# Performance work log

Hardware: AMD Instinct MI355X
Metric: run time of the kernel (lower is better)

## Reference

```python
import jax, jax.numpy as jnp
import numpy as np

N = 100000   # nodes
E = 1600000  # edges
F_IN = 64    # n_features
H = 32       # hidden_size
OUT = 1      # output_size


def _lin(k, fan_in, fan_out):
    return (jax.random.normal(k, (fan_in, fan_out), jnp.float32) / np.sqrt(fan_in)).astype(jnp.float32)


def setup_inputs() -> dict:
    key = jax.random.key(0)
    ks = jax.random.split(key, 16)
    x = jax.random.normal(ks[0], (N, F_IN), jnp.float32)
    edge_index = jax.random.randint(ks[1], (2, E), 0, N, dtype=jnp.int64)
    # guarantee current_node (=0) has outgoing edges so the legal-move mask is non-empty
    edge_index = edge_index.at[0, :64].set(0)
    edge_attr = jax.random.uniform(ks[2], (E,), jnp.float32)
    return {
        "x": x, "edge_index": edge_index, "edge_attr": edge_attr, "current_node": 0,
        # conv_in: GraphConv(F_IN -> H)
        "Win_rel": _lin(ks[3], F_IN, H), "bin_rel": jnp.zeros((H,), jnp.float32), "Win_root": _lin(ks[4], F_IN, H),
        # conv_hidden: GraphConv(H -> H)
        "Wh_rel": _lin(ks[5], H, H), "bh_rel": jnp.zeros((H,), jnp.float32), "Wh_root": _lin(ks[6], H, H),
        # policy_conv: GraphConv(H -> OUT)
        "Wp_rel": _lin(ks[7], H, OUT), "bp_rel": jnp.zeros((OUT,), jnp.float32), "Wp_root": _lin(ks[8], H, OUT),
        # value_conv: GraphConv(H -> OUT)
        "Wv_rel": _lin(ks[9], H, OUT), "bv_rel": jnp.zeros((OUT,), jnp.float32), "Wv_root": _lin(ks[10], H, OUT),
    }


def _graph_conv(h, src, dst, ew, W_rel, b_rel, W_root):
    # PyG GraphConv: out_i = W_root h_i + W_rel * sum_{j->i} e_ji * h_j + b
    msg = h[src] * ew[:, None]                              # [E, d] gather + scale
    agg = jax.ops.segment_sum(msg, dst, num_segments=N)      # [N, d] scatter-add
    return agg @ W_rel + b_rel + h @ W_root


def reference(x, edge_index, edge_attr, current_node,
              Win_rel, bin_rel, Win_root,
              Wh_rel, bh_rel, Wh_root,
              Wp_rel, bp_rel, Wp_root,
              Wv_rel, bv_rel, Wv_root):
    src, dst = edge_index[0], edge_index[1]
    h = jax.nn.relu(_graph_conv(x, src, dst, edge_attr, Win_rel, bin_rel, Win_root))
    h = jax.nn.relu(_graph_conv(h, src, dst, edge_attr, Wh_rel, bh_rel, Wh_root))
    p = _graph_conv(h, src, dst, edge_attr, Wp_rel, bp_rel, Wp_root)  # [N, 1]
    v = _graph_conv(h, src, dst, edge_attr, Wv_rel, bv_rel, Wv_root)  # [N, 1]
    # illegal_moves_mask: 1 for nodes directly reachable from current_node
    hit = (src == current_node).astype(jnp.float32)
    mask = (jnp.zeros((N,), jnp.float32).at[dst].add(hit) > 0).astype(jnp.float32)
    p_m = mask * p.T                                   # [1, N]
    p_m = jnp.where(p_m == 0, -jnp.inf, p_m)
    p_soft = jax.nn.softmax(p_m, axis=1)
    v_m = mask * v.T                                   # [1, N]
    return p_soft.reshape(-1), v_m.reshape(-1)
```

## Files before the change

### kernel.cpp

```cpp
#include <hip/hip_runtime.h>
#include <hip/hip_fp16.h>
#include <cmath>

static constexpr int NN = 100000;
static constexpr int NE = 1600000;
static const size_t NW = (size_t)NN * 32;
static constexpr int SUB = 256;
static constexpr int NSUB = 391;
static constexpr int CH = 8192;
static constexpr int NCH = (NE + CH - 1) / CH;
static constexpr int BCAP = 5200;
static constexpr int CSRN = NSUB * BCAP;
static constexpr int MCAP = 4096;

__device__ __forceinline__ float ent_w(unsigned e)
{
    return __half2float(__ushort_as_half((unsigned short)(e >> 17)));
}
__device__ __forceinline__ int ent_s(unsigned e)
{
    int s = (int)(e & 0x1FFFF);
    return s < NN ? s : NN - 1;
}

__device__ __forceinline__ float4 pack8(const float* v)
{
    union { __half2 h2[4]; float4 f4; } u;
    u.h2[0] = __floats2half2_rn(v[0], v[1]);
    u.h2[1] = __floats2half2_rn(v[2], v[3]);
    u.h2[2] = __floats2half2_rn(v[4], v[5]);
    u.h2[3] = __floats2half2_rn(v[6], v[7]);
    return u.f4;
}

__global__ void __launch_bounds__(512) fused_build_mm1_k(
    const int* __restrict__ src, const int* __restrict__ dst,
    const float* __restrict__ ew, const int* __restrict__ curp,
    int* __restrict__ maskb, int* __restrict__ mcount, int* __restrict__ mlist,
    int* __restrict__ bcnt, uint2* __restrict__ buckets,
    const float* __restrict__ x, const float* __restrict__ Wrel,
    const float* __restrict__ Wroot, const float* __restrict__ bin,
    __half* __restrict__ proj1, __half* __restrict__ root1)
{
    __shared__ union {
        struct {
            uint2 sBuf[CH];
            int lhist[NSUB];
            int lpos[NSUB];
            int lstart[NSUB];
            int lbase[NSUB];
            int tscan[512];
        } s;
        struct {
            float sX[128 * 65];
            float sW[64 * 68];
        } m;
    } u;

    int t = threadIdx.x;
    int bid = blockIdx.x;

    if (bid < NCH) {
        for (int i = t; i < NSUB; i += 512) { u.s.lhist[i] = 0; u.s.lpos[i] = 0; }
        __syncthreads();
        int c0 = bid * CH;
        int cur = curp[0];
        uint2 rent[CH / 512];
        int rb[CH / 512];
#pragma unroll
        for (int it = 0; it < CH / 512; ++it) {
            int e = c0 + it * 512 + t;
            rb[it] = -1;
            if (e < NE) {
                int d = dst[e];
                int sv = src[e];
                if ((unsigned)d < (unsigned)NN) {
                    rb[it] = d >> 8;
                    unsigned bits = __half_as_ushort(__float2half(ew[e]));
                    rent[it].x = ((unsigned)sv & 0x1FFFF) | (bits << 17);
                    rent[it].y = (unsigned)d;
                    atomicAdd(&u.s.lhist[rb[it]], 1);
                    if (sv == cur) {
                        if (atomicExch(maskb + d, 1) == 0) {
                            int idx = atomicAdd(mcount, 1);
                            if (idx < MCAP) mlist[idx] = d;
                        }
                    }
                }
            }
        }
        __syncthreads();
        int v = (t < NSUB) ? u.s.lhist[t] : 0;
        u.s.tscan[t] = v;
        __syncthreads();
        for (int sh = 1; sh < 512; sh <<= 1) {
            int xv = u.s.tscan[t];
            int a = (t >= sh) ? u.s.tscan[t - sh] : 0;
            __syncthreads();
            u.s.tscan[t] = xv + a;
            __syncthreads();
        }
        if (t < NSUB) {
            u.s.lstart[t] = u.s.tscan[t] - v;
            u.s.lbase[t] = (v > 0) ? atomicAdd(&bcnt[t], v) : 0;
        }
        __syncthreads();
#pragma unroll
        for (int it = 0; it < CH / 512; ++it) {
            if (rb[it] >= 0) {
                int p = atomicAdd(&u.s.lpos[rb[it]], 1);
                u.s.sBuf[u.s.lstart[rb[it]] + p] = rent[it];
            }
        }
        __syncthreads();
        int total = u.s.lstart[NSUB - 1] + u.s.lhist[NSUB - 1];
        for (int j = t; j < total; j += 512) {
            uint2 en = u.s.sBuf[j];
            int b = (int)(en.y >> 8);
            if (b >= NSUB) b = NSUB - 1;
            unsigned pos = (unsigned)(u.s.lbase[b] + (j - u.s.lstart[b]));
            if (pos < (unsigned)BCAP) buckets[(size_t)b * BCAP + pos] = en;
        }
    } else {
        int mb = bid - NCH;
        for (int i = t; i < 64 * 32; i += 512) {
            int k = i >> 5, j = i & 31;
            u.m.sW[k * 68 + j] = Wrel[i];
            u.m.sW[k * 68 + 32 + j] = Wroot[i];
        }
        int base = mb * 128;
        for (int i = t; i < 2048; i += 512) {
            int node = i >> 4;
            int k = (i & 15) * 4;
            int n = base + node;
            if (n >= NN) n = NN - 1;
            float4 v4 = *(const float4*)(x + (size_t)n * 64 + k);
            float* p = u.m.sX + node * 65 + k;
            p[0] = v4.x; p[1] = v4.y; p[2] = v4.z; p[3] = v4.w;
        }
        __syncthreads();
        int cg = t & 7;
        int ng = t >> 3;
        int c0m = 8 * cg;
        float acc[2][8] = {};
        for (int k = 0; k < 64; ++k) {
            float xv0 = u.m.sX[(2 * ng + 0) * 65 + k];
            float xv1 = u.m.sX[(2 * ng + 1) * 65 + k];
            float4 w0 = *(const float4*)(u.m.sW + k * 68 + c0m);
            float4 w1 = *(const float4*)(u.m.sW + k * 68 + c0m + 4);
            const float* wp = (const float*)&w0;
#pragma unroll
            for (int j = 0; j < 4; ++j) {
                float w = wp[j];
                acc[0][j] = fmaf(xv0, w, acc[0][j]);
                acc[1][j] = fmaf(xv1, w, acc[1][j]);
            }
            const float* wq = (const float*)&w1;
#pragma unroll
            for (int j = 0; j < 4; ++j) {
                float w = wq[j];
                acc[0][4 + j] = fmaf(xv0, w, acc[0][4 + j]);
                acc[1][4 + j] = fmaf(xv1, w, acc[1][4 + j]);
            }
        }
#pragma unroll
        for (int r = 0; r < 2; ++r) {
            int n = base + 2 * ng + r;
            if (n >= NN) break;
            if (cg < 4) {
                *(float4*)(proj1 + (size_t)n * 32 + c0m) = pack8(acc[r]);
            } else {
                int c = c0m - 32;
                float vv[8];
#pragma unroll
                for (int j = 0; j < 8; ++j) vv[j] = acc[r][j] + bin[c + j];
                *(float4*)(root1 + (size_t)n * 32 + c) = pack8(vv);
            }
        }
    }
}

__global__ void __launch_bounds__(512) sortB_k(
    const uint2* __restrict__ buckets, const int* __restrict__ bcnt,
    unsigned* __restrict__ csr4, int* __restrict__ deg, int* __restrict__ off)
{
    __shared__ uint2 sBuf[BCAP];
    __shared__ int lhist[SUB];
    __shared__ int lstart[SUB];
    __shared__ int lcur[SUB];
    __shared__ int tscan[256];
    int g = blockIdx.x, t = threadIdx.x;
    if (t < SUB) { lhist[t] = 0; lcur[t] = 0; }
    __syncthreads();
    int cnt = bcnt[g];
    if (cnt < 0) cnt = 0;
    if (cnt > BCAP) cnt = BCAP;
    const uint2* bk = buckets + (size_t)g * BCAP;
    for (int i = t; i < cnt; i += 512) {
        uint2 e = bk[i];
        sBuf[i] = e;
        atomicAdd(&lhist[e.y & (SUB - 1)], 1);
    }
    __syncthreads();
    if (t < 256) tscan[t] = lhist[t];
    __syncthreads();
    for (int s = 1; s < 256; s <<= 1) {
        int x = 0, a = 0;
        if (t < 256) { x = tscan[t]; a = (t >= s) ? tscan[t - s] : 0; }
        __syncthreads();
        if (t < 256) tscan[t] = x + a;
        __syncthreads();
    }
    if (t < 256) lstart[t] = tscan[t] - lhist[t];
    __syncthreads();
    int base = g * BCAP;
    for (int i = t; i < cnt; i += 512) {
        uint2 e = sBuf[i];
        int ld = (int)(e.y & (SUB - 1));
        int p = atomicAdd(&lcur[ld], 1);
        unsigned pos = (unsigned)(base + lstart[ld] + p);
        if (pos < (unsigned)CSRN) csr4[pos] = e.x;
    }
    if (t < SUB) {
        int n = g * SUB + t;
        if (n < NN) {
            deg[n] = lhist[t];
            off[n] = base + lstart[t];
        }
    }
}

__global__ void __launch_bounds__(256) mm2_k(
    const __half* __restrict__ h1, const float* __restrict__ Wrel,
    const float* __restrict__ Wroot, const float* __restrict__ bh,
    __half* __restrict__ proj2, __half* __restrict__ root2)
{
    __shared__ float sX[128 * 33];
    __shared__ float sW[32 * 68];
    int t = threadIdx.x;
    for (int i = t; i < 32 * 32; i += 256) {
        int k = i >> 5, j = i & 31;
        sW[k * 68 + j] = Wrel[i];
        sW[k * 68 + 32 + j] = Wroot[i];
    }
    int base = blockIdx.x * 128;
    for (int i = t; i < 512; i += 256) {
        int node = i >> 2;
        int hs = (i & 3) * 8;
        int n = base + node;
        if (n >= NN) n = NN - 1;
        float4 v = *(const float4*)(h1 + (size_t)n * 32 + hs);
        const __half2* hp = (const __half2*)&v;
        float* p = sX + node * 33 + hs;
#pragma unroll
        for (int u = 0; u < 4; ++u) {
            float2 f2 = __half22float2(hp[u]);
            p[2 * u] = f2.x;
            p[2 * u + 1] = f2.y;
        }
    }
    __syncthreads();
    int cg = t & 7;
    int ng = t >> 3;
    int c0 = 8 * cg;
    float acc[4][8] = {};
    for (int k = 0; k < 32; ++k) {
        float xv0 = sX[(4 * ng + 0) * 33 + k];
        float xv1 = sX[(4 * ng + 1) * 33 + k];
        float xv2 = sX[(4 * ng + 2) * 33 + k];
        float xv3 = sX[(4 * ng + 3) * 33 + k];
        float4 w0 = *(const float4*)(sW + k * 68 + c0);
        float4 w1 = *(const float4*)(sW + k * 68 + c0 + 4);
        const float* wp = (const float*)&w0;
#pragma unroll
        for (int j = 0; j < 4; ++j) {
            float w = wp[j];
            acc[0][j] = fmaf(xv0, w, acc[0][j]);
            acc[1][j] = fmaf(xv1, w, acc[1][j]);
            acc[2][j] = fmaf(xv2, w, acc[2][j]);
            acc[3][j] = fmaf(xv3, w, acc[3][j]);
        }
        const float* wq = (const float*)&w1;
#pragma unroll
        for (int j = 0; j < 4; ++j) {
            float w = wq[j];
            acc[0][4 + j] = fmaf(xv0, w, acc[0][4 + j]);
            acc[1][4 + j] = fmaf(xv1, w, acc[1][4 + j]);
            acc[2][4 + j] = fmaf(xv2, w, acc[2][4 + j]);
            acc[3][4 + j] = fmaf(xv3, w, acc[3][4 + j]);
        }
    }
#pragma unroll
    for (int r = 0; r < 4; ++r) {
        int n = base + 4 * ng + r;
        if (n >= NN) break;
        if (cg < 4) {
            *(float4*)(proj2 + (size_t)n * 32 + c0) = pack8(acc[r]);
        } else {
            int c = c0 - 32;
            float v[8];
#pragma unroll
            for (int j = 0; j < 8; ++j) v[j] = acc[r][j] + bh[c + j];
            *(float4*)(root2 + (size_t)n * 32 + c) = pack8(v);
        }
    }
}

__global__ void __launch_bounds__(256) agg1_v4(
    const __half* __restrict__ proj1, const __half* __restrict__ root1,
    const unsigned* __restrict__ csr4, const int* __restrict__ off,
    const int* __restrict__ deg, __half* __restrict__ h1)
{
    int t = threadIdx.x;
    int q = t & 3;
    int f0 = q * 8;
    int n = blockIdx.x * 64 + (t >> 2);
    if (n >= NN) return;
    int st = off[n];
    int dg = deg[n];
    if (st < 0) st = 0;
    if (st > CSRN) st = CSRN;
    if (dg < 0) dg = 0;
    if (dg > CSRN - st) dg = CSRN - st;
    float acc[8] = {0.f, 0.f, 0.f, 0.f, 0.f, 0.f, 0.f, 0.f};
    int i = 0;
    for (; i + 1 < dg; i += 2) {
        unsigned e0 = csr4[st + i];
        unsigned e1 = csr4[st + i + 1];
        float w0 = ent_w(e0), w1 = ent_w(e1);
        float4 r0 = *(const float4*)(proj1 + (size_t)ent_s(e0) * 32 + f0);
        float4 r1 = *(const float4*)(proj1 + (size_t)ent_s(e1) * 32 + f0);
        const __half2* h0 = (const __half2*)&r0;
        const __half2* h1p = (const __half2*)&r1;
#pragma unroll
        for (int u = 0; u < 4; ++u) {
            float2 a = __half22float2(h0[u]);
            float2 b = __half22float2(h1p[u]);
            acc[2 * u] = fmaf(w0, a.x, acc[2 * u]);
            acc[2 * u + 1] = fmaf(w0, a.y, acc[2 * u + 1]);
            acc[2 * u] = fmaf(w1, b.x, acc[2 * u]);
            acc[2 * u + 1] = fmaf(w1, b.y, acc[2 * u + 1]);
        }
    }
    if (i < dg) {
        unsigned e0 = csr4[st + i];
        float w0 = ent_w(e0);
        float4 r0 = *(const float4*)(proj1 + (size_t)ent_s(e0) * 32 + f0);
        const __half2* h0 = (const __half2*)&r0;
#pragma unroll
        for (int u = 0; u < 4; ++u) {
            float2 a = __half22float2(h0[u]);
            acc[2 * u] = fmaf(w0, a.x, acc[2 * u]);
            acc[2 * u + 1] = fmaf(w0, a.y, acc[2 * u + 1]);
        }
    }
    float4 rr = *(const float4*)(root1 + (size_t)n * 32 + f0);
    const __half2* rp = (const __half2*)&rr;
    float h[8];
#pragma unroll
    for (int u = 0; u < 4; ++u) {
        float2 f2 = __half22float2(rp[u]);
        h[2 * u] = fmaxf(acc[2 * u] + f2.x, 0.f);
        h[2 * u + 1] = fmaxf(acc[2 * u + 1] + f2.y, 0.f);
    }
    *(float4*)(h1 + (size_t)n * 32 + f0) = pack8(h);
}

__global__ void __launch_bounds__(256) agg2_v4(
    const __half* __restrict__ proj2, const __half* __restrict__ root2,
    const float* __restrict__ Wp_rel, const float* __restrict__ Wp_root,
    const float* __restrict__ bp, const float* __restrict__ Wv_rel,
    const float* __restrict__ Wv_root, const float* __restrict__ bv,
    const unsigned* __restrict__ csr4, const int* __restrict__ off,
    const int* __restrict__ deg, float2* __restrict__ pv,
    float* __restrict__ pbase, float* __restrict__ vbase,
    float* __restrict__ out_p, float* __restrict__ out_v)
{
    __shared__ float sHead[4 * 32];
    if (threadIdx.x < 32) {
        sHead[threadIdx.x] = Wp_rel[threadIdx.x];
        sHead[32 + threadIdx.x] = Wp_root[threadIdx.x];
        sHead[64 + threadIdx.x] = Wv_rel[threadIdx.x];
        sHead[96 + threadIdx.x] = Wv_root[threadIdx.x];
    }
    __syncthreads();
    int t = threadIdx.x;
    int q = t & 3;
    int f0 = q * 8;
    int n = blockIdx.x * 64 + (t >> 2);
    if (n >= NN) return;
    int st = off[n];
    int dg = deg[n];
    if (st < 0) st = 0;
    if (st > CSRN) st = CSRN;
    if (dg < 0) dg = 0;
    if (dg > CSRN - st) dg = CSRN - st;
    float acc[8] = {0.f, 0.f, 0.f, 0.f, 0.f, 0.f, 0.f, 0.f};
    int i = 0;
    for (; i + 1 < dg; i += 2) {
        unsigned e0 = csr4[st + i];
        unsigned e1 = csr4[st + i + 1];
        float w0 = ent_w(e0), w1 = ent_w(e1);
        float4 r0 = *(const float4*)(proj2 + (size_t)ent_s(e0) * 32 + f0);
        float4 r1 = *(const float4*)(proj2 + (size_t)ent_s(e1) * 32 + f0);
        const __half2* h0 = (const __half2*)&r0;
        const __half2* h1p = (const __half2*)&r1;
#pragma unroll
        for (int u = 0; u < 4; ++u) {
            float2 a = __half22float2(h0[u]);
            float2 b = __half22float2(h1p[u]);
            acc[2 * u] = fmaf(w0, a.x, acc[2 * u]);
            acc[2 * u + 1] = fmaf(w0, a.y, acc[2 * u + 1]);
            acc[2 * u] = fmaf(w1, b.x, acc[2 * u]);
            acc[2 * u + 1] = fmaf(w1, b.y, acc[2 * u + 1]);
        }
    }
    if (i < dg) {
        unsigned e0 = csr4[st + i];
        float w0 = ent_w(e0);
        float4 r0 = *(const float4*)(proj2 + (size_t)ent_s(e0) * 32 + f0);
        const __half2* h0 = (const __half2*)&r0;
#pragma unroll
        for (int u = 0; u < 4; ++u) {
            float2 a = __half22float2(h0[u]);
            acc[2 * u] = fmaf(w0, a.x, acc[2 * u]);
            acc[2 * u + 1] = fmaf(w0, a.y, acc[2 * u + 1]);
        }
    }
    float4 rr = *(const float4*)(root2 + (size_t)n * 32 + f0);
    const __half2* rp = (const __half2*)&rr;
    float h[8];
#pragma unroll
    for (int u = 0; u < 4; ++u) {
        float2 f2 = __half22float2(rp[u]);
        h[2 * u] = fmaxf(acc[2 * u] + f2.x, 0.f);
        h[2 * u + 1] = fmaxf(acc[2 * u + 1] + f2.y, 0.f);
    }
    float prv = 0.f, pov = 0.f, vrv = 0.f, vov = 0.f;
#pragma unroll
    for (int j = 0; j < 8; ++j) {
        prv = fmaf(h[j], sHead[f0 + j], prv);
        pov = fmaf(h[j], sHead[32 + f0 + j], pov);
        vrv = fmaf(h[j], sHead[64 + f0 + j], vrv);
        vov = fmaf(h[j], sHead[96 + f0 + j], vov);
    }
#pragma unroll
    for (int m = 1; m <= 2; m <<= 1) {
        prv += __shfl_xor(prv, m, 64);
        pov += __shfl_xor(pov, m, 64);
        vrv += __shfl_xor(vrv, m, 64);
        vov += __shfl_xor(vov, m, 64);
    }
    if (q == 0) {
        pv[n] = make_float2(prv, vrv);
        pbase[n] = pov + bp[0];
        vbase[n] = vov + bv[0];
        out_p[n] = 0.f;
        out_v[n] = 0.f;
    }
}

__global__ void __launch_bounds__(256) masked_softmax_k(
    const int* __restrict__ mlist, const int* __restrict__ mcount,
    const unsigned* __restrict__ csr4, const int* __restrict__ off,
    const int* __restrict__ deg, const float2* __restrict__ pv,
    const float* __restrict__ pbase, const float* __restrict__ vbase,
    float* __restrict__ out_p, float* __restrict__ out_v)
{
    __shared__ float sPm[MCAP];
    __shared__ float sV[MCAP];
    __shared__ int sN[MCAP];
    __shared__ float sMx, sSum;
    __shared__ float sred[4];
    int m = mcount[0];
    if (m > MCAP) m = MCAP;
    if (m < 0) m = 0;
    for (int idx = threadIdx.x; idx < m; idx += 256) {
        int n = mlist[idx];
        if ((unsigned)n >= (unsigned)NN) n = 0;
        sN[idx] = n;
        int st = off[n];
        int dg = deg[n];
        if (st < 0) st = 0;
        if (st > CSRN) st = CSRN;
        if (dg < 0) dg = 0;
        if (dg > CSRN - st) dg = CSRN - st;
        float pa = 0.f, va = 0.f;
        for (int i = 0; i < dg; ++i) {
            unsigned ent = csr4[st + i];
            int s = ent_s(ent);
            float w = ent_w(ent);
            float2 tv = pv[s];
            pa = fmaf(tv.x, w, pa);
            va = fmaf(tv.y, w, va);
        }
        float p = pa + pbase[n];
        sPm[idx] = (p == 0.f) ? -INFINITY : p;
        sV[idx] = va + vbase[n];
    }
    __syncthreads();
    float mx = -INFINITY;
    for (int i = threadIdx.x; i < m; i += 256) mx = fmaxf(mx, sPm[i]);
#pragma unroll
    for (int k = 32; k; k >>= 1) mx = fmaxf(mx, __shfl_xor(mx, k, 64));
    if ((threadIdx.x & 63) == 0) sred[threadIdx.x >> 6] = mx;
    __syncthreads();
    if (threadIdx.x == 0)
        sMx = fmaxf(fmaxf(sred[0], sred[1]), fmaxf(sred[2], sred[3]));
    __syncthreads();
    float sum = 0.f;
    for (int i = threadIdx.x; i < m; i += 256) {
        float x = sPm[i];
        sum += (x == -INFINITY) ? 0.f : expf(x - sMx);
    }
#pragma unroll
    for (int k = 32; k; k >>= 1) sum += __shfl_xor(sum, k, 64);
    if ((threadIdx.x & 63) == 0) sred[threadIdx.x >> 6] = sum;
    __syncthreads();
    if (threadIdx.x == 0) sSum = sred[0] + sred[1] + sred[2] + sred[3];
    __syncthreads();
    for (int idx = threadIdx.x; idx < m; idx += 256) {
        int n = sN[idx];
        float x = sPm[idx];
        out_p[n] = (x == -INFINITY) ? 0.f : expf(x - sMx) / sSum;
        out_v[n] = sV[idx];
    }
}

extern "C" void kernel_launch(void* const* d_in, const int* in_sizes, int n_in,
                              void* d_out, int out_size, void* d_ws,
                              size_t ws_size, hipStream_t stream)
{
    const float* x        = (const float*)d_in[0];
    const int*   ei       = (const int*)d_in[1];
    const float* ew       = (const float*)d_in[2];
    const int*   cur      = (const int*)d_in[3];
    const float* Win_rel  = (const float*)d_in[4];
    const float* bin_rel  = (const float*)d_in[5];
    const float* Win_root = (const float*)d_in[6];
    const float* Wh_rel   = (const float*)d_in[7];
    const float* bh_rel   = (const float*)d_in[8];
    const float* Wh_root  = (const float*)d_in[9];
    const float* Wp_rel   = (const float*)d_in[10];
    const float* bp       = (const float*)d_in[11];
    const float* Wp_root  = (const float*)d_in[12];
    const float* Wv_rel   = (const float*)d_in[13];
    const float* bv       = (const float*)d_in[14];
    const float* Wv_root  = (const float*)d_in[15];

    const int* srcA = ei;
    const int* dstA = ei + NE;

    char* w8 = (char*)d_ws;
    unsigned* csr4 = (unsigned*)w8;
    int* deg    = (int*)(csr4 + CSRN);
    int* off    = deg + NN;
    int* maskb  = off + NN;
    int* mcount = maskb + NN;
    int* bcnt   = mcount + 8;
    int* mlist  = bcnt + 400;
    __half* proj1 = (__half*)(mlist + MCAP);
    __half* root1 = proj1 + NW;
    __half* h1    = root1 + NW;
    __half* proj2 = h1 + NW;
    __half* root2 = proj2 + NW;
    float2* pv    = (float2*)(root2 + NW);
    float* pbase  = (float*)(pv + NN);
    float* vbase  = pbase + NN;
    uint2* buckets = (uint2*)(vbase + NN);

    float* out_p = (float*)d_out;
    float* out_v = out_p + NN;

    const int NB_MM    = (NN + 127) / 128;
    const int NB_AGG   = (NN + 63) / 64;
    const int NB_FUSED = NCH + NB_MM;

    hipMemsetAsync(maskb, 0, ((size_t)NN + 8 + 400) * sizeof(int), stream);

    fused_build_mm1_k<<<NB_FUSED, 512, 0, stream>>>(
        srcA, dstA, ew, cur, maskb, mcount, mlist, bcnt, buckets,
        x, Win_rel, Win_root, bin_rel, proj1, root1);
    sortB_k<<<NSUB, 512, 0, stream>>>(buckets, bcnt, csr4, deg, off);

    agg1_v4<<<NB_AGG, 256, 0, stream>>>(proj1, root1, csr4, off, deg, h1);
    mm2_k<<<NB_MM, 256, 0, stream>>>(h1, Wh_rel, Wh_root, bh_rel, proj2, root2);
    agg2_v4<<<NB_AGG, 256, 0, stream>>>(proj2, root2, Wp_rel, Wp_root, bp,
                                        Wv_rel, Wv_root, bv, csr4, off, deg,
                                        pv, pbase, vbase, out_p, out_v);
    masked_softmax_k<<<1, 256, 0, stream>>>(mlist, mcount, csr4, off, deg, pv,
                                            pbase, vbase, out_p, out_v);
}
```

Measured before the change: 248.5 us.

## Drop CSR sort; aggregate from buckets via shared-memory atomics and fuse agg1 with mm2

Removes the sortB CSR-construction kernel. The two aggregation passes now read the per-256-node buckets directly and accumulate into shared memory with atomics. Layer-1 aggregation, ReLU and the hidden-layer matmul are fused into one kernel, which drops the h1 round-trip. The masked policy/value sums are computed by a bucket-scan kernel that skips slices with no masked nodes, and the chunk size drops to 4096. The cost is heavy shared-memory atomic traffic and only 391 blocks per aggregation pass, which limits parallelism.

```diff
diff --git a/kernel.cpp b/kernel.cpp
--- a/kernel.cpp
+++ b/kernel.cpp
@@ -7,10 +7,9 @@
 static const size_t NW = (size_t)NN * 32;
 static constexpr int SUB = 256;
 static constexpr int NSUB = 391;
-static constexpr int CH = 8192;
+static constexpr int CH = 4096;
 static constexpr int NCH = (NE + CH - 1) / CH;
 static constexpr int BCAP = 5200;
-static constexpr int CSRN = NSUB * BCAP;
 static constexpr int MCAP = 4096;
 
 __device__ __forceinline__ float ent_w(unsigned e)
@@ -37,7 +36,8 @@
     const int* __restrict__ src, const int* __restrict__ dst,
     const float* __restrict__ ew, const int* __restrict__ curp,
     int* __restrict__ maskb, int* __restrict__ mcount, int* __restrict__ mlist,
-    int* __restrict__ bcnt, uint2* __restrict__ buckets,
+    int* __restrict__ mslice, int* __restrict__ bcnt,
+    uint2* __restrict__ buckets,
     const float* __restrict__ x, const float* __restrict__ Wrel,
     const float* __restrict__ Wroot, const float* __restrict__ bin,
     __half* __restrict__ proj1, __half* __restrict__ root1)
@@ -84,6 +84,7 @@
                         if (atomicExch(maskb + d, 1) == 0) {
                             int idx = atomicAdd(mcount, 1);
                             if (idx < MCAP) mlist[idx] = d;
+                            mslice[d >> 8] = 1;
                         }
                     }
                 }
@@ -180,290 +181,269 @@
     }
 }
 
-__global__ void __launch_bounds__(512) sortB_k(
+__global__ void __launch_bounds__(512) agg1_mm2_k(
     const uint2* __restrict__ buckets, const int* __restrict__ bcnt,
-    unsigned* __restrict__ csr4, int* __restrict__ deg, int* __restrict__ off)
-{
-    __shared__ uint2 sBuf[BCAP];
-    __shared__ int lhist[SUB];
-    __shared__ int lstart[SUB];
-    __shared__ int lcur[SUB];
-    __shared__ int tscan[256];
+    const __half* __restrict__ proj1, const __half* __restrict__ root1,
+    const float* __restrict__ Wrel, const float* __restrict__ Wroot,
+    const float* __restrict__ bh,
+    __half* __restrict__ proj2, __half* __restrict__ root2)
+{
+    __shared__ float acc[SUB * 33];
+    __shared__ float sW[32 * 68];
     int g = blockIdx.x, t = threadIdx.x;
-    if (t < SUB) { lhist[t] = 0; lcur[t] = 0; }
+    for (int i = t; i < SUB * 33; i += 512) acc[i] = 0.f;
+    for (int i = t; i < 32 * 32; i += 512) {
+        int k = i >> 5, j = i & 31;
+        sW[k * 68 + j] = Wrel[i];
+        sW[k * 68 + 32 + j] = Wroot[i];
+    }
     __syncthreads();
     int cnt = bcnt[g];
     if (cnt < 0) cnt = 0;
     if (cnt > BCAP) cnt = BCAP;
     const uint2* bk = buckets + (size_t)g * BCAP;
-    for (int i = t; i < cnt; i += 512) {
-        uint2 e = bk[i];
-        sBuf[i] = e;
-        atomicAdd(&lhist[e.y & (SUB - 1)], 1);
-    }
-    __syncthreads();
-    if (t < 256) tscan[t] = lhist[t];
-    __syncthreads();
-    for (int s = 1; s < 256; s <<= 1) {
-        int x = 0, a = 0;
-        if (t < 256) { x = tscan[t]; a = (t >= s) ? tscan[t - s] : 0; }
-        __syncthreads();
-        if (t < 256) tscan[t] = x + a;
-        __syncthreads();
-    }
-    if (t < 256) lstart[t] = tscan[t] - lhist[t];
-    __syncthreads();
-    int base = g * BCAP;
-    for (int i = t; i < cnt; i += 512) {
-        uint2 e = sBuf[i];
-        int ld = (int)(e.y & (SUB - 1));
-        int p = atomicAdd(&lcur[ld], 1);
-        unsigned pos = (unsigned)(base + lstart[ld] + p);
-        if (pos < (unsigned)CSRN) csr4[pos] = e.x;
-    }
-    if (t < SUB) {
-        int n = g * SUB + t;
+    int q = t & 3, f0 = q * 8;
+    int i = t >> 2;
+    for (; i + 128 < cnt; i += 256) {
+        uint2 e0 = bk[i];
+        uint2 e1 = bk[i + 128];
+        float w0 = ent_w(e0.x), w1 = ent_w(e1.x);
+        float4 r0 = *(const float4*)(proj1 + (size_t)ent_s(e0.x) * 32 + f0);
+        float4 r1 = *(const float4*)(proj1 + (size_t)ent_s(e1.x) * 32 + f0);
+        float* a0 = acc + (int)(e0.y & 255) * 33 + f0;
+        float* a1 = acc + (int)(e1.y & 255) * 33 + f0;
+        const __half2* h0 = (const __half2*)&r0;
+        const __half2* h1p = (const __half2*)&r1;
+#pragma unroll
+        for (int u2 = 0; u2 < 4; ++u2) {
+            float2 a = __half22float2(h0[u2]);
+            atomicAdd(a0 + 2 * u2, w0 * a.x);
+            atomicAdd(a0 + 2 * u2 + 1, w0 * a.y);
+        }
+#pragma unroll
+        for (int u2 = 0; u2 < 4; ++u2) {
+            float2 b = __half22float2(h1p[u2]);
+            atomicAdd(a1 + 2 * u2, w1 * b.x);
+            atomicAdd(a1 + 2 * u2 + 1, w1 * b.y);
+        }
+    }
+    if (i < cnt) {
+        uint2 e0 = bk[i];
+        float w0 = ent_w(e0.x);
+        float4 r0 = *(const float4*)(proj1 + (size_t)ent_s(e0.x) * 32 + f0);
+        float* a0 = acc + (int)(e0.y & 255) * 33 + f0;
+        const __half2* h0 = (const __half2*)&r0;
+#pragma unroll
+        for (int u2 = 0; u2 < 4; ++u2) {
+            float2 a = __half22float2(h0[u2]);
+            atomicAdd(a0 + 2 * u2, w0 * a.x);
+            atomicAdd(a0 + 2 * u2 + 1, w0 * a.y);
+        }
+    }
+    __syncthreads();
+    {
+        int l = t >> 1, fb = (t & 1) * 16;
+        int n = g * SUB + l;
         if (n < NN) {
-            deg[n] = lhist[t];
-            off[n] = base + lstart[t];
-        }
-    }
-}
-
-__global__ void __launch_bounds__(256) mm2_k(
-    const __half* __restrict__ h1, const float* __restrict__ Wrel,
-    const float* __restrict__ Wroot, const float* __restrict__ bh,
-    __half* __restrict__ proj2, __half* __restrict__ root2)
-{
-    __shared__ float sX[128 * 33];
-    __shared__ float sW[32 * 68];
-    int t = threadIdx.x;
-    for (int i = t; i < 32 * 32; i += 256) {
-        int k = i >> 5, j = i & 31;
-        sW[k * 68 + j] = Wrel[i];
-        sW[k * 68 + 32 + j] = Wroot[i];
-    }
-    int base = blockIdx.x * 128;
-    for (int i = t; i < 512; i += 256) {
-        int node = i >> 2;
-        int hs = (i & 3) * 8;
-        int n = base + node;
-        if (n >= NN) n = NN - 1;
-        float4 v = *(const float4*)(h1 + (size_t)n * 32 + hs);
-        const __half2* hp = (const __half2*)&v;
-        float* p = sX + node * 33 + hs;
-#pragma unroll
-        for (int u = 0; u < 4; ++u) {
-            float2 f2 = __half22float2(hp[u]);
-            p[2 * u] = f2.x;
-            p[2 * u + 1] = f2.y;
-        }
-    }
-    __syncthreads();
-    int cg = t & 7;
-    int ng = t >> 3;
-    int c0 = 8 * cg;
-    float acc[4][8] = {};
+            float4 ra = *(const float4*)(root1 + (size_t)n * 32 + fb);
+            float4 rb = *(const float4*)(root1 + (size_t)n * 32 + fb + 8);
+            const __half2* pa = (const __half2*)&ra;
+            const __half2* pb = (const __half2*)&rb;
+            float* ap = acc + l * 33 + fb;
+#pragma unroll
+            for (int u2 = 0; u2 < 4; ++u2) {
+                float2 f2 = __half22float2(pa[u2]);
+                ap[2 * u2] = fmaxf(ap[2 * u2] + f2.x, 0.f);
+                ap[2 * u2 + 1] = fmaxf(ap[2 * u2 + 1] + f2.y, 0.f);
+            }
+#pragma unroll
+            for (int u2 = 0; u2 < 4; ++u2) {
+                float2 f2 = __half22float2(pb[u2]);
+                ap[8 + 2 * u2] = fmaxf(ap[8 + 2 * u2] + f2.x, 0.f);
+                ap[8 + 2 * u2 + 1] = fmaxf(ap[8 + 2 * u2 + 1] + f2.y, 0.f);
+            }
+        }
+    }
+    __syncthreads();
+    int cg = t & 7, ng = t >> 3, c0 = 8 * cg;
+    float a2[4][8] = {};
     for (int k = 0; k < 32; ++k) {
-        float xv0 = sX[(4 * ng + 0) * 33 + k];
-        float xv1 = sX[(4 * ng + 1) * 33 + k];
-        float xv2 = sX[(4 * ng + 2) * 33 + k];
-        float xv3 = sX[(4 * ng + 3) * 33 + k];
+        float x0 = acc[(4 * ng + 0) * 33 + k];
+        float x1 = acc[(4 * ng + 1) * 33 + k];
+        float x2 = acc[(4 * ng + 2) * 33 + k];
+        float x3 = acc[(4 * ng + 3) * 33 + k];
         float4 w0 = *(const float4*)(sW + k * 68 + c0);
         float4 w1 = *(const float4*)(sW + k * 68 + c0 + 4);
         const float* wp = (const float*)&w0;
 #pragma unroll
         for (int j = 0; j < 4; ++j) {
             float w = wp[j];
-            acc[0][j] = fmaf(xv0, w, acc[0][j]);
-            acc[1][j] = fmaf(xv1, w, acc[1][j]);
-            acc[2][j] = fmaf(xv2, w, acc[2][j]);
-            acc[3][j] = fmaf(xv3, w, acc[3][j]);
+            a2[0][j] = fmaf(x0, w, a2[0][j]);
+            a2[1][j] = fmaf(x1, w, a2[1][j]);
+            a2[2][j] = fmaf(x2, w, a2[2][j]);
+            a2[3][j] = fmaf(x3, w, a2[3][j]);
         }
         const float* wq = (const float*)&w1;
 #pragma unroll
         for (int j = 0; j < 4; ++j) {
             float w = wq[j];
-            acc[0][4 + j] = fmaf(xv0, w, acc[0][4 + j]);
-            acc[1][4 + j] = fmaf(xv1, w, acc[1][4 + j]);
-            acc[2][4 + j] = fmaf(xv2, w, acc[2][4 + j]);
-            acc[3][4 + j] = fmaf(xv3, w, acc[3][4 + j]);
+            a2[0][4 + j] = fmaf(x0, w, a2[0][4 + j]);
+            a2[1][4 + j] = fmaf(x1, w, a2[1][4 + j]);
+            a2[2][4 + j] = fmaf(x2, w, a2[2][4 + j]);
+            a2[3][4 + j] = fmaf(x3, w, a2[3][4 + j]);
         }
     }
 #pragma unroll
     for (int r = 0; r < 4; ++r) {
-        int n = base + 4 * ng + r;
+        int n = g * SUB + 4 * ng + r;
         if (n >= NN) break;
         if (cg < 4) {
-            *(float4*)(proj2 + (size_t)n * 32 + c0) = pack8(acc[r]);
+            *(float4*)(proj2 + (size_t)n * 32 + c0) = pack8(a2[r]);
         } else {
             int c = c0 - 32;
-            float v[8];
-#pragma unroll
-            for (int j = 0; j < 8; ++j) v[j] = acc[r][j] + bh[c + j];
-            *(float4*)(root2 + (size_t)n * 32 + c) = pack8(v);
-        }
-    }
-}
-
-__global__ void __launch_bounds__(256) agg1_v4(
-    const __half* __restrict__ proj1, const __half* __restrict__ root1,
-    const unsigned* __restrict__ csr4, const int* __restrict__ off,
-    const int* __restrict__ deg, __half* __restrict__ h1)
-{
-    int t = threadIdx.x;
-    int q = t & 3;
-    int f0 = q * 8;
-    int n = blockIdx.x * 64 + (t >> 2);
-    if (n >= NN) return;
-    int st = off[n];
-    int dg = deg[n];
-    if (st < 0) st = 0;
-    if (st > CSRN) st = CSRN;
-    if (dg < 0) dg = 0;
-    if (dg > CSRN - st) dg = CSRN - st;
-    float acc[8] = {0.f, 0.f, 0.f, 0.f, 0.f, 0.f, 0.f, 0.f};
-    int i = 0;
-    for (; i + 1 < dg; i += 2) {
-        unsigned e0 = csr4[st + i];
-        unsigned e1 = csr4[st + i + 1];
-        float w0 = ent_w(e0), w1 = ent_w(e1);
-        float4 r0 = *(const float4*)(proj1 + (size_t)ent_s(e0) * 32 + f0);
-        float4 r1 = *(const float4*)(proj1 + (size_t)ent_s(e1) * 32 + f0);
-        const __half2* h0 = (const __half2*)&r0;
-        const __half2* h1p = (const __half2*)&r1;
-#pragma unroll
-        for (int u = 0; u < 4; ++u) {
-            float2 a = __half22float2(h0[u]);
-            float2 b = __half22float2(h1p[u]);
-            acc[2 * u] = fmaf(w0, a.x, acc[2 * u]);
-            acc[2 * u + 1] = fmaf(w0, a.y, acc[2 * u + 1]);
-            acc[2 * u] = fmaf(w1, b.x, acc[2 * u]);
-            acc[2 * u + 1] = fmaf(w1, b.y, acc[2 * u + 1]);
-        }
-    }
-    if (i < dg) {
-        unsigned e0 = csr4[st + i];
-        float w0 = ent_w(e0);
-        float4 r0 = *(const float4*)(proj1 + (size_t)ent_s(e0) * 32 + f0);
-        const __half2* h0 = (const __half2*)&r0;
-#pragma unroll
-        for (int u = 0; u < 4; ++u) {
-            float2 a = __half22float2(h0[u]);
-            acc[2 * u] = fmaf(w0, a.x, acc[2 * u]);
-            acc[2 * u + 1] = fmaf(w0, a.y, acc[2 * u + 1]);
-        }
-    }
-    float4 rr = *(const float4*)(root1 + (size_t)n * 32 + f0);
-    const __half2* rp = (const __half2*)&rr;
-    float h[8];
-#pragma unroll
-    for (int u = 0; u < 4; ++u) {
-        float2 f2 = __half22float2(rp[u]);
-        h[2 * u] = fmaxf(acc[2 * u] + f2.x, 0.f);
-        h[2 * u + 1] = fmaxf(acc[2 * u + 1] + f2.y, 0.f);
-    }
-    *(float4*)(h1 + (size_t)n * 32 + f0) = pack8(h);
-}
-
-__global__ void __launch_bounds__(256) agg2_v4(
+            float vv[8];
+#pragma unroll
+            for (int j = 0; j < 8; ++j) vv[j] = a2[r][j] + bh[c + j];
+            *(float4*)(root2 + (size_t)n * 32 + c) = pack8(vv);
+        }
+    }
+}
+
+__global__ void __launch_bounds__(512) agg2_k(
+    const uint2* __restrict__ buckets, const int* __restrict__ bcnt,
     const __half* __restrict__ proj2, const __half* __restrict__ root2,
     const float* __restrict__ Wp_rel, const float* __restrict__ Wp_root,
     const float* __restrict__ bp, const float* __restrict__ Wv_rel,
     const float* __restrict__ Wv_root, const float* __restrict__ bv,
-    const unsigned* __restrict__ csr4, const int* __restrict__ off,
-    const int* __restrict__ deg, float2* __restrict__ pv,
-    float* __restrict__ pbase, float* __restrict__ vbase,
-    float* __restrict__ out_p, float* __restrict__ out_v)
-{
+    float2* __restrict__ pv, float* __restrict__ pbase,
+    float* __restrict__ vbase, float* __restrict__ out_p,
+    float* __restrict__ out_v)
+{
+    __shared__ float acc[SUB * 33];
     __shared__ float sHead[4 * 32];
-    if (threadIdx.x < 32) {
-        sHead[threadIdx.x] = Wp_rel[threadIdx.x];
-        sHead[32 + threadIdx.x] = Wp_root[threadIdx.x];
-        sHead[64 + threadIdx.x] = Wv_rel[threadIdx.x];
-        sHead[96 + threadIdx.x] = Wv_root[threadIdx.x];
-    }
-    __syncthreads();
-    int t = threadIdx.x;
-    int q = t & 3;
-    int f0 = q * 8;
-    int n = blockIdx.x * 64 + (t >> 2);
-    if (n >= NN) return;
-    int st = off[n];
-    int dg = deg[n];
-    if (st < 0) st = 0;
-    if (st > CSRN) st = CSRN;
-    if (dg < 0) dg = 0;
-    if (dg > CSRN - st) dg = CSRN - st;
-    float acc[8] = {0.f, 0.f, 0.f, 0.f, 0.f, 0.f, 0.f, 0.f};
-    int i = 0;
-    for (; i + 1 < dg; i += 2) {
-        unsigned e0 = csr4[st + i];
-        unsigned e1 = csr4[st + i + 1];
-        float w0 = ent_w(e0), w1 = ent_w(e1);
-        float4 r0 = *(const float4*)(proj2 + (size_t)ent_s(e0) * 32 + f0);
-        float4 r1 = *(const float4*)(proj2 + (size_t)ent_s(e1) * 32 + f0);
+    int g = blockIdx.x, t = threadIdx.x;
+    for (int i = t; i < SUB * 33; i += 512) acc[i] = 0.f;
+    if (t < 32) {
+        sHead[t] = Wp_rel[t];
+        sHead[32 + t] = Wp_root[t];
+        sHead[64 + t] = Wv_rel[t];
+        sHead[96 + t] = Wv_root[t];
+    }
+    __syncthreads();
+    int cnt = bcnt[g];
+    if (cnt < 0) cnt = 0;
+    if (cnt > BCAP) cnt = BCAP;
+    const uint2* bk = buckets + (size_t)g * BCAP;
+    int q = t & 3, f0 = q * 8;
+    int i = t >> 2;
+    for (; i + 128 < cnt; i += 256) {
+        uint2 e0 = bk[i];
+        uint2 e1 = bk[i + 128];
+        float w0 = ent_w(e0.x), w1 = ent_w(e1.x);
+        float4 r0 = *(const float4*)(proj2 + (size_t)ent_s(e0.x) * 32 + f0);
+        float4 r1 = *(const float4*)(proj2 + (size_t)ent_s(e1.x) * 32 + f0);
+        float* a0 = acc + (int)(e0.y & 255) * 33 + f0;
+        float* a1 = acc + (int)(e1.y & 255) * 33 + f0;
         const __half2* h0 = (const __half2*)&r0;
         const __half2* h1p = (const __half2*)&r1;
 #pragma unroll
-        for (int u = 0; u < 4; ++u) {
-            float2 a = __half22float2(h0[u]);
-            float2 b = __half22float2(h1p[u]);
-            acc[2 * u] = fmaf(w0, a.x, acc[2 * u]);
-            acc[2 * u + 1] = fmaf(w0, a.y, acc[2 * u + 1]);
-            acc[2 * u] = fmaf(w1, b.x, acc[2 * u]);
-            acc[2 * u + 1] = fmaf(w1, b.y, acc[2 * u + 1]);
-        }
-    }
-    if (i < dg) {
-        unsigned e0 = csr4[st + i];
-        float w0 = ent_w(e0);
-        float4 r0 = *(const float4*)(proj2 + (size_t)ent_s(e0) * 32 + f0);
+        for (int u2 = 0; u2 < 4; ++u2) {
+            float2 a = __half22float2(h0[u2]);
+            atomicAdd(a0 + 2 * u2, w0 * a.x);
+            atomicAdd(a0 + 2 * u2 + 1, w0 * a.y);
+        }
+#pragma unroll
+        for (int u2 = 0; u2 < 4; ++u2) {
+            float2 b = __half22float2(h1p[u2]);
+            atomicAdd(a1 + 2 * u2, w1 * b.x);
+            atomicAdd(a1 + 2 * u2 + 1, w1 * b.y);
+        }
+    }
+    if (i < cnt) {
+        uint2 e0 = bk[i];
+        float w0 = ent_w(e0.x);
+        float4 r0 = *(const float4*)(proj2 + (size_t)ent_s(e0.x) * 32 + f0);
+        float* a0 = acc + (int)(e0.y & 255) * 33 + f0;
         const __half2* h0 = (const __half2*)&r0;
 #pragma unroll
-        for (int u = 0; u < 4; ++u) {
-            float2 a = __half22float2(h0[u]);
-            acc[2 * u] = fmaf(w0, a.x, acc[2 * u]);
-            acc[2 * u + 1] = fmaf(w0, a.y, acc[2 * u + 1]);
-        }
-    }
-    float4 rr = *(const float4*)(root2 + (size_t)n * 32 + f0);
-    const __half2* rp = (const __half2*)&rr;
-    float h[8];
-#pragma unroll
-    for (int u = 0; u < 4; ++u) {
-        float2 f2 = __half22float2(rp[u]);
-        h[2 * u] = fmaxf(acc[2 * u] + f2.x, 0.f);
-        h[2 * u + 1] = fmaxf(acc[2 * u + 1] + f2.y, 0.f);
-    }
-    float prv = 0.f, pov = 0.f, vrv = 0.f, vov = 0.f;
-#pragma unroll
-    for (int j = 0; j < 8; ++j) {
-        prv = fmaf(h[j], sHead[f0 + j], prv);
-        pov = fmaf(h[j], sHead[32 + f0 + j], pov);
-        vrv = fmaf(h[j], sHead[64 + f0 + j], vrv);
-        vov = fmaf(h[j], sHead[96 + f0 + j], vov);
-    }
-#pragma unroll
-    for (int m = 1; m <= 2; m <<= 1) {
-        prv += __shfl_xor(prv, m, 64);
-        pov += __shfl_xor(pov, m, 64);
-        vrv += __shfl_xor(vrv, m, 64);
-        vov += __shfl_xor(vov, m, 64);
-    }
-    if (q == 0) {
-        pv[n] = make_float2(prv, vrv);
-        pbase[n] = pov + bp[0];
-        vbase[n] = vov + bv[0];
-        out_p[n] = 0.f;
-        out_v[n] = 0.f;
+        for (int u2 = 0; u2 < 4; ++u2) {
+            float2 a = __half22float2(h0[u2]);
+            atomicAdd(a0 + 2 * u2, w0 * a.x);
+            atomicAdd(a0 + 2 * u2 + 1, w0 * a.y);
+        }
+    }
+    __syncthreads();
+    int l = t >> 1, fb = (t & 1) * 16;
+    int n = g * SUB + l;
+    if (n < NN) {
+        float4 ra = *(const float4*)(root2 + (size_t)n * 32 + fb);
+        float4 rb = *(const float4*)(root2 + (size_t)n * 32 + fb + 8);
+        const __half2* pa = (const __half2*)&ra;
+        const __half2* pb = (const __half2*)&rb;
+        const float* ap = acc + l * 33 + fb;
+        float h[16];
+#pragma unroll
+        for (int u2 = 0; u2 < 4; ++u2) {
+            float2 f2 = __half22float2(pa[u2]);
+            h[2 * u2] = fmaxf(ap[2 * u2] + f2.x, 0.f);
+            h[2 * u2 + 1] = fmaxf(ap[2 * u2 + 1] + f2.y, 0.f);
+        }
+#pragma unroll
+        for (int u2 = 0; u2 < 4; ++u2) {
+            float2 f2 = __half22float2(pb[u2]);
+            h[8 + 2 * u2] = fmaxf(ap[8 + 2 * u2] + f2.x, 0.f);
+            h[8 + 2 * u2 + 1] = fmaxf(ap[8 + 2 * u2 + 1] + f2.y, 0.f);
+        }
+        float pr = 0.f, po = 0.f, vr = 0.f, vo = 0.f;
+#pragma unroll
+        for (int j = 0; j < 16; ++j) {
+            int f = fb + j;
+            pr = fmaf(h[j], sHead[f], pr);
+            po = fmaf(h[j], sHead[32 + f], po);
+            vr = fmaf(h[j], sHead[64 + f], vr);
+            vo = fmaf(h[j], sHead[96 + f], vo);
+        }
+        pr += __shfl_xor(pr, 1, 64);
+        po += __shfl_xor(po, 1, 64);
+        vr += __shfl_xor(vr, 1, 64);
+        vo += __shfl_xor(vo, 1, 64);
+        if ((t & 1) == 0) {
+            pv[n] = make_float2(pr, vr);
+            pbase[n] = po + bp[0];
+            vbase[n] = vo + bv[0];
+            out_p[n] = 0.f;
+            out_v[n] = 0.f;
+        }
+    }
+}
+
+__global__ void __launch_bounds__(256) masked_pv_k(
+    const uint2* __restrict__ buckets, const int* __restrict__ bcnt,
+    const int* __restrict__ mslice, const int* __restrict__ maskb,
+    const float2* __restrict__ pv, float* __restrict__ pacc,
+    float* __restrict__ vacc)
+{
+    int g = blockIdx.x;
+    if (mslice[g] == 0) return;
+    int cnt = bcnt[g];
+    if (cnt < 0) cnt = 0;
+    if (cnt > BCAP) cnt = BCAP;
+    const uint2* bk = buckets + (size_t)g * BCAP;
+    for (int i = threadIdx.x; i < cnt; i += 256) {
+        uint2 e = bk[i];
+        unsigned d = e.y;
+        if (d < (unsigned)NN && maskb[d] != 0) {
+            float w = ent_w(e.x);
+            float2 tv = pv[ent_s(e.x)];
+            atomicAdd(pacc + d, w * tv.x);
+            atomicAdd(vacc + d, w * tv.y);
+        }
     }
 }
 
 __global__ void __launch_bounds__(256) masked_softmax_k(
     const int* __restrict__ mlist, const int* __restrict__ mcount,
-    const unsigned* __restrict__ csr4, const int* __restrict__ off,
-    const int* __restrict__ deg, const float2* __restrict__ pv,
+    const float* __restrict__ pacc, const float* __restrict__ vacc,
     const float* __restrict__ pbase, const float* __restrict__ vbase,
     float* __restrict__ out_p, float* __restrict__ out_v)
 {
@@ -479,24 +459,9 @@
         int n = mlist[idx];
         if ((unsigned)n >= (unsigned)NN) n = 0;
         sN[idx] = n;
-        int st = off[n];
-        int dg = deg[n];
-        if (st < 0) st = 0;
-        if (st > CSRN) st = CSRN;
-        if (dg < 0) dg = 0;
-        if (dg > CSRN - st) dg = CSRN - st;
-        float pa = 0.f, va = 0.f;
-        for (int i = 0; i < dg; ++i) {
-            unsigned ent = csr4[st + i];
-            int s = ent_s(ent);
-            float w = ent_w(ent);
-            float2 tv = pv[s];
-            pa = fmaf(tv.x, w, pa);
-            va = fmaf(tv.y, w, va);
-        }
-        float p = pa + pbase[n];
+        float p = pacc[n] + pbase[n];
         sPm[idx] = (p == 0.f) ? -INFINITY : p;
-        sV[idx] = va + vbase[n];
+        sV[idx] = vacc[n] + vbase[n];
     }
     __syncthreads();
     float mx = -INFINITY;
@@ -552,17 +517,16 @@
     const int* dstA = ei + NE;
 
     char* w8 = (char*)d_ws;
-    unsigned* csr4 = (unsigned*)w8;
-    int* deg    = (int*)(csr4 + CSRN);
-    int* off    = deg + NN;
-    int* maskb  = off + NN;
+    int* maskb  = (int*)w8;
     int* mcount = maskb + NN;
     int* bcnt   = mcount + 8;
-    int* mlist  = bcnt + 400;
+    int* mslice = bcnt + 400;
+    float* pacc = (float*)(mslice + 400);
+    float* vacc = pacc + NN;
+    int* mlist  = (int*)(vacc + NN);
     __half* proj1 = (__half*)(mlist + MCAP);
     __half* root1 = proj1 + NW;
-    __half* h1    = root1 + NW;
-    __half* proj2 = h1 + NW;
+    __half* proj2 = root1 + NW;
     __half* root2 = proj2 + NW;
     float2* pv    = (float2*)(root2 + NW);
     float* pbase  = (float*)(pv + NN);
@@ -573,21 +537,21 @@
     float* out_v = out_p + NN;
 
     const int NB_MM    = (NN + 127) / 128;
-    const int NB_AGG   = (NN + 63) / 64;
     const int NB_FUSED = NCH + NB_MM;
 
-    hipMemsetAsync(maskb, 0, ((size_t)NN + 8 + 400) * sizeof(int), stream);
+    hipMemsetAsync(maskb, 0, ((size_t)NN * 3 + 8 + 800) * sizeof(int), stream);
 
     fused_build_mm1_k<<<NB_FUSED, 512, 0, stream>>>(
-        srcA, dstA, ew, cur, maskb, mcount, mlist, bcnt, buckets,
+        srcA, dstA, ew, cur, maskb, mcount, mlist, mslice, bcnt, buckets,
         x, Win_rel, Win_root, bin_rel, proj1, root1);
-    sortB_k<<<NSUB, 512, 0, stream>>>(buckets, bcnt, csr4, deg, off);
-
-    agg1_v4<<<NB_AGG, 256, 0, stream>>>(proj1, root1, csr4, off, deg, h1);
-    mm2_k<<<NB_MM, 256, 0, stream>>>(h1, Wh_rel, Wh_root, bh_rel, proj2, root2);
-    agg2_v4<<<NB_AGG, 256, 0, stream>>>(proj2, root2, Wp_rel, Wp_root, bp,
-                                        Wv_rel, Wv_root, bv, csr4, off, deg,
-                                        pv, pbase, vbase, out_p, out_v);
-    masked_softmax_k<<<1, 256, 0, stream>>>(mlist, mcount, csr4, off, deg, pv,
+    agg1_mm2_k<<<NSUB, 512, 0, stream>>>(buckets, bcnt, proj1, root1,
+                                         Wh_rel, Wh_root, bh_rel,
+                                         proj2, root2);
+    agg2_k<<<NSUB, 512, 0, stream>>>(buckets, bcnt, proj2, root2,
+                                     Wp_rel, Wp_root, bp, Wv_rel, Wv_root, bv,
+                                     pv, pbase, vbase, out_p, out_v);
+    masked_pv_k<<<NSUB, 256, 0, stream>>>(buckets, bcnt, mslice, maskb, pv,
+                                          pacc, vacc);
+    masked_softmax_k<<<1, 256, 0, stream>>>(mlist, mcount, pacc, vacc,
                                             pbase, vbase, out_p, out_v);
 }
```

New measurement: 862.0 us. 247% more time.
